# Kernel tuning notes

Hardware: AMD Instinct MI355X
Metric: run time of the kernel (lower is better)

The kernel has to match this reference:

```python
import jax, jax.numpy as jnp
import numpy as np

HIDDEN = 300
N_HEADS = 4
DEPTH = 4
N_ATOMS = 30000
N_BONDS = 60000
MAX_NB = 6
N_MOLS = 600
ATOMS_PER_MOL = 50
ATOM_FDIM = 144
BOND_IN = ATOM_FDIM + 14  # 158
W_SCALE = 0.05


def setup_inputs() -> dict:
    key = jax.random.key(0)
    ks = jax.random.split(key, 12)
    rn = lambda k, shp: jax.random.normal(k, shp, dtype=jnp.float32)
    return {
        'fatoms': rn(ks[0], (N_ATOMS, ATOM_FDIM)),
        'fbonds': rn(ks[1], (N_BONDS, BOND_IN)),
        'agraph': jax.random.randint(ks[2], (N_ATOMS, MAX_NB), 0, N_BONDS, dtype=jnp.int32),
        'bgraph': jax.random.randint(ks[3], (N_BONDS, MAX_NB), 0, N_BONDS, dtype=jnp.int32),
        'W_i': rn(ks[4], (HIDDEN, BOND_IN)) * W_SCALE,
        'W_ma': rn(ks[5], (N_HEADS, HIDDEN, HIDDEN)) * W_SCALE,
        'W_h': rn(ks[6], (HIDDEN, N_HEADS * HIDDEN)) * W_SCALE,
        'W_o': rn(ks[7], (HIDDEN, ATOM_FDIM + HIDDEN)) * W_SCALE,
        'b_o': rn(ks[8], (HIDDEN,)) * W_SCALE,
        'W_a': rn(ks[9], (HIDDEN, HIDDEN)) * W_SCALE,
        'W_b': rn(ks[10], (HIDDEN, HIDDEN)) * W_SCALE,
        'b_b': rn(ks[11], (HIDDEN,)) * W_SCALE,
    }


def reference(fatoms, fbonds, agraph, bgraph, W_i, W_ma, W_h, W_o, b_o, W_a, W_b, b_b):
    E, K = bgraph.shape
    NH = W_ma.shape[0]
    H = W_i.shape[0]

    binput = fbonds @ W_i.T                      # [E, H]
    message = jax.nn.relu(binput)
    for _ in range(DEPTH - 1):
        nei = message[bgraph]                    # [E, K, H] gather over neighbor bonds
        # per-head attention scores: <W_ma[n] @ nei_ek, message_e>
        mt = jnp.einsum('eh,nhd->ned', message, W_ma)        # [NH, E, H]
        scores = jnp.einsum('ekd,ned->nek', nei, mt)         # [NH, E, K]
        w = jax.nn.softmax(scores, axis=2)
        comp = jnp.einsum('nek,ekh->enh', w, nei)            # [E, NH, H]
        nei_msg = comp.reshape(E, NH * H) @ W_h.T            # [E, H]
        message = jax.nn.relu(binput + nei_msg)              # dropout(p=0) = identity

    a_nei = message[agraph].sum(axis=1)          # [A, H] gather-sum incoming bonds
    ainput = jnp.concatenate([fatoms, a_nei], axis=1)
    atom_hiddens = jax.nn.relu(ainput @ W_o.T + b_o)         # [A, H]

    # uniform scope: N_MOLS molecules of ATOMS_PER_MOL atoms each
    cur = atom_hiddens.reshape(N_MOLS, ATOMS_PER_MOL, H)
    att_w = jax.nn.softmax(jnp.einsum('mah,mbh->mab', cur @ W_a.T, cur), axis=2)
    att_h = jax.nn.relu(jnp.einsum('mab,mbh->mah', att_w, cur) @ W_b.T + b_b)
    mol_vecs = (cur + att_h).sum(axis=1) / ATOMS_PER_MOL     # [N_MOLS, H]
    return mol_vecs
```

## Files before the change

kernel.cpp:

```cpp
#include <hip/hip_runtime.h>
#include <hip/hip_bf16.h>
#include <math.h>

#define HID       300
#define HP        320
#define NH        4
#define E_BONDS   60000
#define NATOMS    30000
#define KNB       6
#define NMOLS     600
#define APM       50
#define AFD       144
#define BONDIN    158

typedef unsigned short u16;
typedef unsigned int   u32;
typedef _Float16 f16;
typedef f16   f16x8 __attribute__((ext_vector_type(8)));
typedef float f32x4 __attribute__((ext_vector_type(4)));

__device__ inline float hlo(u32 u) { union { u32 i; f16 h[2]; } c; c.i = u; return (float)c.h[0]; }
__device__ inline float hhi(u32 u) { union { u32 i; f16 h[2]; } c; c.i = u; return (float)c.h[1]; }
__device__ inline u32 packh2(float a, float b) {
    union { u32 i; f16 h[2]; } c; c.h[0] = (f16)a; c.h[1] = (f16)b; return c.i;
}

__device__ inline void gl2lds16(const void* g, void* l) {
    __builtin_amdgcn_global_load_lds(
        (const __attribute__((address_space(1))) void*)g,
        (__attribute__((address_space(3))) void*)l, 16, 0, 0);
}

template <int BN, int EPI>
__global__ __launch_bounds__(256, 4) void mfma_gemm_k(
    const f16* __restrict__ A, int lda,
    const f16* __restrict__ B, int ldb,
    int M, int Nb, int K, int ldc,
    int nbx, int mby,
    float* __restrict__ Cf, f16* __restrict__ Ch,
    const float* __restrict__ bias,
    const f16* __restrict__ resid,
    f16* __restrict__ out2)
{
    constexpr int NF = BN / 32;
    __shared__ f16 sA[128 * 64];
    __shared__ f16 sB[BN * 64];
    const int b    = blockIdx.x;
    const int xcd  = b & 7;
    const int q    = b >> 3;
    const int xb   = q % nbx;
    const int yb   = (q / nbx) * 8 + xcd;
    if (yb >= mby) return;
    const int tid  = threadIdx.x;
    const int lane = tid & 63;
    const int wv   = tid >> 6;
    const int wm   = wv >> 1, wn = wv & 1;
    const int m0   = yb * 128, n0 = xb * BN;

    f32x4 acc[4][NF];
#pragma unroll
    for (int i = 0; i < 4; ++i)
#pragma unroll
        for (int j = 0; j < NF; ++j) acc[i][j] = (f32x4){0.f, 0.f, 0.f, 0.f};

    for (int k0 = 0; k0 < K; k0 += 64) {
        __syncthreads();
#pragma unroll
        for (int i = 0; i < 4; ++i) {
            int o   = (((i * 4 + wv) * 64) + lane) * 16;
            int row = o >> 7;
            int p   = (o >> 4) & 7;
            int gr  = m0 + row; gr = gr < M ? gr : M - 1;
            const f16* g = A + (size_t)gr * lda + k0 + ((p ^ (row & 7)) << 3);
            gl2lds16(g, (char*)sA + (i * 4 + wv) * 1024);
        }
#pragma unroll
        for (int i = 0; i < BN / 32; ++i) {
            int o   = (((i * 4 + wv) * 64) + lane) * 16;
            int row = o >> 7;
            int p   = (o >> 4) & 7;
            int gr  = n0 + row; gr = gr < Nb ? gr : Nb - 1;
            const f16* g = B + (size_t)gr * ldb + k0 + ((p ^ (row & 7)) << 3);
            gl2lds16(g, (char*)sB + (i * 4 + wv) * 1024);
        }
        __syncthreads();

        const int rl = lane & 15, cl = lane >> 4;
#pragma unroll
        for (int kh = 0; kh < 2; ++kh) {
            f16x8 af[4], bfr[NF];
#pragma unroll
            for (int mf = 0; mf < 4; ++mf) {
                int row = wm * 64 + mf * 16 + rl;
                int ch  = (kh * 4 + cl) ^ (row & 7);
                af[mf]  = *(const f16x8*)&sA[row * 64 + ch * 8];
            }
#pragma unroll
            for (int nf = 0; nf < NF; ++nf) {
                int row = wn * (BN / 2) + nf * 16 + rl;
                int ch  = (kh * 4 + cl) ^ (row & 7);
                bfr[nf] = *(const f16x8*)&sB[row * 64 + ch * 8];
            }
#pragma unroll
            for (int mf = 0; mf < 4; ++mf)
#pragma unroll
                for (int nf = 0; nf < NF; ++nf)
                    acc[mf][nf] = __builtin_amdgcn_mfma_f32_16x16x32_f16(
                        af[mf], bfr[nf], acc[mf][nf], 0, 0, 0);
        }
    }

    const int rl = lane & 15, cl = lane >> 4;
#pragma unroll
    for (int mf = 0; mf < 4; ++mf) {
#pragma unroll
        for (int r = 0; r < 4; ++r) {
            int gm = m0 + wm * 64 + mf * 16 + cl * 4 + r;
            if (gm >= M) continue;
#pragma unroll
            for (int nf = 0; nf < NF; ++nf) {
                int gn = n0 + wn * (BN / 2) + nf * 16 + rl;
                if (gn >= ldc) continue;
                float v = acc[mf][nf][r];
                size_t ci = (size_t)gm * ldc + gn;
                if (EPI == 0) {
                    Cf[ci] = v;
                } else if (EPI == 1) {
                    Ch[ci] = (f16)v;
                } else if (EPI == 2) {
                    Ch[ci] = (f16)v;
                    out2[ci] = (f16)fmaxf(v, 0.f);
                } else if (EPI == 3) {
                    v += (float)resid[ci];
                    Ch[ci] = (f16)fmaxf(v, 0.f);
                } else if (EPI == 4) {
                    v += Cf[ci];
                    v += (gn < HID) ? bias[gn] : 0.f;
                    v = fmaxf(v, 0.f);
                    Cf[ci] = v; Ch[ci] = (f16)v;
                } else if (EPI == 5) {
                    v += (gn < HID) ? bias[gn] : 0.f;
                    Cf[ci] = fmaxf(v, 0.f);
                } else {
                    v += (gn < HID) ? bias[gn] : 0.f;
                    Ch[ci] = (f16)fmaxf(v, 0.f);
                }
            }
        }
    }
}

static inline int swz_grid(int nbx, int mby) { return nbx * 8 * ((mby + 7) / 8); }

__global__ __launch_bounds__(256) void score_comp_k(
    const f16* __restrict__ msg,
    f16* __restrict__ mtc,
    const int* __restrict__ bgraph)
{
    const int tid = threadIdx.x;
    const int e   = blockIdx.x * 16 + (tid >> 4);
    const int t   = tid & 15;

    u32 nei[KNB][10];
#pragma unroll
    for (int k = 0; k < KNB; ++k) {
        int nb = bgraph[e * KNB + k];
        const u32* p = (const u32*)(msg + (size_t)nb * HP) + t * 10;
#pragma unroll
        for (int j = 0; j < 10; ++j) nei[k][j] = p[j];
    }

    for (int n = 0; n < NH; ++n) {
        u32* mrow = (u32*)(mtc + (size_t)e * (NH * HP) + n * HP) + t * 10;
        u32 mt[10];
#pragma unroll
        for (int j = 0; j < 10; ++j) mt[j] = mrow[j];

        float pk[KNB] = {0.f, 0.f, 0.f, 0.f, 0.f, 0.f};
#pragma unroll
        for (int j = 0; j < 10; ++j) {
            float m0 = hlo(mt[j]), m1 = hhi(mt[j]);
#pragma unroll
            for (int k = 0; k < KNB; ++k)
                pk[k] += hlo(nei[k][j]) * m0 + hhi(nei[k][j]) * m1;
        }
#pragma unroll
        for (int s = 1; s < 16; s <<= 1)
#pragma unroll
            for (int k = 0; k < KNB; ++k) pk[k] += __shfl_xor(pk[k], s);

        float mx = pk[0];
#pragma unroll
        for (int k = 1; k < KNB; ++k) mx = fmaxf(mx, pk[k]);
        float w[KNB], sum = 0.f;
#pragma unroll
        for (int k = 0; k < KNB; ++k) { w[k] = __expf(pk[k] - mx); sum += w[k]; }
        float inv = 1.f / sum;
#pragma unroll
        for (int k = 0; k < KNB; ++k) w[k] *= inv;

#pragma unroll
        for (int j = 0; j < 10; ++j) {
            float c0 = 0.f, c1 = 0.f;
#pragma unroll
            for (int k = 0; k < KNB; ++k) {
                c0 += w[k] * hlo(nei[k][j]);
                c1 += w[k] * hhi(nei[k][j]);
            }
            mrow[j] = packh2(c0, c1);
        }
    }
}

__global__ void gather_sum_h_k(const f16* __restrict__ msg,
                               const int* __restrict__ agraph,
                               f16* __restrict__ out512) {
    int idx = blockIdx.x * 256 + threadIdx.x;
    if (idx >= NATOMS * (HP / 2)) return;
    int a = idx / (HP / 2), c = idx - a * (HP / 2);
    const int* g = agraph + (size_t)a * KNB;
    float s0 = 0.f, s1 = 0.f;
#pragma unroll
    for (int k = 0; k < KNB; ++k) {
        u32 u = *(const u32*)(msg + (size_t)g[k] * HP + c * 2);
        s0 += hlo(u); s1 += hhi(u);
    }
    ((u32*)out512)[(size_t)a * 256 + 96 + c] = packh2(s0, s1);
}

__global__ void conv_pad_k(const float* __restrict__ src, f16* __restrict__ dst,
                           int R, int C, int CP, int RP) {
    int idx = blockIdx.x * 256 + threadIdx.x;
    if (idx >= R * CP) return;
    int r = idx / CP, c = idx - r * CP;
    dst[(size_t)r * RP + c] = (f16)(c < C ? src[(size_t)r * C + c] : 0.f);
}

__global__ void prep_w_k(const float* __restrict__ src, f16* __restrict__ dst,
                         int mode, int R, int CK) {
    int idx = blockIdx.x * 256 + threadIdx.x;
    if (idx >= R * CK) return;
    int r = idx / CK, c = idx - r * CK;
    float v = 0.f;
    if (mode == 0) {
        if (r < HID && c < BONDIN) v = src[r * BONDIN + c];
    } else if (mode == 1) {
        int n = r / HP, d = r - n * HP;
        if (d < HID && c < HID) v = src[((size_t)n * HID + c) * HID + d];
    } else if (mode == 2) {
        int n = c / HP, d = c - n * HP;
        if (r < HID && d < HID) v = src[(size_t)r * (NH * HID) + n * HID + d];
    } else if (mode == 7) {
        if (r < HID) {
            if (c < AFD) v = src[r * (AFD + HID) + c];
            else if (c >= 192 && c < 192 + HID) v = src[r * (AFD + HID) + AFD + (c - 192)];
        }
    } else {
        if (r < HID && c < HID) v = src[r * HID + c];
    }
    dst[idx] = (f16)v;
}

__global__ __launch_bounds__(256) void mol_attn_mfma_k(
    const f16* __restrict__ atomHh,
    const f16* __restrict__ ah2h,
    f16* __restrict__ comp2h)
{
    __shared__ f16 sCur[64 * 320];
    __shared__ float sP[64][66];
    const int tid  = threadIdx.x;
    const int lane = tid & 63;
    const int wv   = tid >> 6;
    const int m    = blockIdx.x;
    const int rl   = lane & 15, cl = lane >> 4;

#pragma unroll
    for (int i = 0; i < 10; ++i) {
        int g   = i * 256 + wv * 64 + lane;
        int row = g / 40, c = g - row * 40;
        int grow = m * APM + row; grow = grow < NATOMS ? grow : NATOMS - 1;
        const f16* src = atomHh + (size_t)grow * HP + ((c ^ (row & 7)) << 3);
        gl2lds16(src, (char*)sCur + (size_t)(i * 256 + wv * 64) * 16);
    }
    __syncthreads();

    f32x4 acc[4];
#pragma unroll
    for (int nf = 0; nf < 4; ++nf) acc[nf] = (f32x4){0.f, 0.f, 0.f, 0.f};
    int qrow = m * APM + wv * 16 + rl;
    qrow = qrow < NATOMS ? qrow : NATOMS - 1;
    const f16* qbase = ah2h + (size_t)qrow * HP;
#pragma unroll
    for (int kh = 0; kh < 10; ++kh) {
        f16x8 aq = *(const f16x8*)(qbase + kh * 32 + cl * 8);
#pragma unroll
        for (int nf = 0; nf < 4; ++nf) {
            int brow = nf * 16 + rl;
            int ch   = (kh * 4 + cl) ^ (brow & 7);
            f16x8 bv = *(const f16x8*)&sCur[brow * 320 + ch * 8];
            acc[nf] = __builtin_amdgcn_mfma_f32_16x16x32_f16(aq, bv, acc[nf], 0, 0, 0);
        }
    }

#pragma unroll
    for (int r = 0; r < 4; ++r) {
        float s[4];
#pragma unroll
        for (int nf = 0; nf < 4; ++nf) {
            s[nf] = acc[nf][r];
            if (nf == 3 && rl >= 2) s[nf] = -1e30f;
        }
        float mx = fmaxf(fmaxf(s[0], s[1]), fmaxf(s[2], s[3]));
#pragma unroll
        for (int msk = 1; msk < 16; msk <<= 1) mx = fmaxf(mx, __shfl_xor(mx, msk));
        float e[4], sum = 0.f;
#pragma unroll
        for (int nf = 0; nf < 4; ++nf) { e[nf] = __expf(s[nf] - mx); sum += e[nf]; }
#pragma unroll
        for (int msk = 1; msk < 16; msk <<= 1) sum += __shfl_xor(sum, msk);
        float inv = 1.f / sum;
        int a = wv * 16 + cl * 4 + r;
#pragma unroll
        for (int nf = 0; nf < 4; ++nf) sP[a][nf * 16 + rl] = e[nf] * inv;
    }
    __syncthreads();

    const int a  = tid >> 2, hq = tid & 3;
    const bool aval = a < APM;
    const size_t orow = (size_t)(m * APM + a) * HP;
#pragma unroll
    for (int p = 0; p < 2; ++p) {
        float av[40];
#pragma unroll
        for (int i = 0; i < 40; ++i) av[i] = 0.f;
        const int ch0 = p * 20 + hq * 5;
        for (int b = 0; b < APM; ++b) {
            float w = sP[a][b];
#pragma unroll
            for (int i = 0; i < 5; ++i) {
                int ch = (ch0 + i) ^ (b & 7);
                f16x8 cv = *(const f16x8*)&sCur[b * 320 + ch * 8];
#pragma unroll
                for (int j = 0; j < 8; ++j) av[i * 8 + j] += w * (float)cv[j];
            }
        }
        if (aval) {
#pragma unroll
            for (int i = 0; i < 5; ++i) {
                f16x8 o;
#pragma unroll
                for (int j = 0; j < 8; ++j) o[j] = (f16)av[i * 8 + j];
                *(f16x8*)&comp2h[orow + p * 160 + hq * 40 + i * 8] = o;
            }
        }
    }
}

__global__ void mol_reduce_k(const f16* __restrict__ atomHh,
                             const f16* __restrict__ atthh,
                             float* __restrict__ out) {
    const int m = blockIdx.x;
    for (int h = threadIdx.x; h < HID; h += 256) {
        float s = 0.f;
        for (int a = 0; a < APM; ++a) {
            size_t i = (size_t)(m * APM + a) * HP + h;
            s += (float)atomHh[i] + (float)atthh[i];
        }
        out[(size_t)m * HID + h] = s * (1.f / APM);
    }
}

extern "C" void kernel_launch(void* const* d_in, const int* in_sizes, int n_in,
                              void* d_out, int out_size, void* d_ws, size_t ws_size,
                              hipStream_t stream) {
    const float* fatoms = (const float*)d_in[0];
    const float* fbonds = (const float*)d_in[1];
    const int*   agraph = (const int*)d_in[2];
    const int*   bgraph = (const int*)d_in[3];
    const float* W_i    = (const float*)d_in[4];
    const float* W_ma   = (const float*)d_in[5];
    const float* W_h    = (const float*)d_in[6];
    const float* W_o    = (const float*)d_in[7];
    const float* b_o    = (const float*)d_in[8];
    const float* W_a    = (const float*)d_in[9];
    const float* W_b    = (const float*)d_in[10];
    const float* b_b    = (const float*)d_in[11];
    float* out = (float*)d_out;

    char* ws = (char*)d_ws;
    f16* fbondsh = (f16*)ws;
    f16* mtall   = (f16*)ws;
    f16* fat512  = (f16*)ws;
    f16* atomHh  = (f16*)(ws + 115200000);
    f16* ah2h    = (f16*)(ws + 134400000);
    f16* comp2h  = (f16*)(ws + 153600000);
    f16* atthh   = (f16*)(ws + 172800000);
    f16* binh    = (f16*)(ws + 153600000);
    f16* msgh    = (f16*)(ws + 192000000);
    char* wb = ws + 230400000;
    f16* WiT   = (f16*)(wb);
    f16* WmaT  = (f16*)(wb + 122880);
    f16* WhT   = (f16*)(wb + 942080);
    f16* Wo512 = (f16*)(wb + 1761280);
    f16* Wa    = (f16*)(wb + 2088960);
    f16* Wb    = (f16*)(wb + 2293760);

    prep_w_k<<<dim3((320 * 192 + 255) / 256), dim3(256), 0, stream>>>(W_i, WiT, 0, 320, 192);
    prep_w_k<<<dim3((1280 * 320 + 255) / 256), dim3(256), 0, stream>>>(W_ma, WmaT, 1, 1280, 320);
    prep_w_k<<<dim3((320 * 1280 + 255) / 256), dim3(256), 0, stream>>>(W_h, WhT, 2, 320, 1280);
    prep_w_k<<<dim3((320 * 512 + 255) / 256), dim3(256), 0, stream>>>(W_o, Wo512, 7, 320, 512);
    prep_w_k<<<dim3((320 * 320 + 255) / 256), dim3(256), 0, stream>>>(W_a, Wa, 5, 320, 320);
    prep_w_k<<<dim3((320 * 320 + 255) / 256), dim3(256), 0, stream>>>(W_b, Wb, 6, 320, 320);
    conv_pad_k<<<dim3((E_BONDS * 192 + 255) / 256), dim3(256), 0, stream>>>(
        fbonds, fbondsh, E_BONDS, BONDIN, 192, 192);

    mfma_gemm_k<128, 2><<<dim3(swz_grid(3, 469)), dim3(256), 0, stream>>>(
        fbondsh, 192, WiT, 192, E_BONDS, 320, 192, HP, 3, 469,
        nullptr, binh, nullptr, nullptr, msgh);

    for (int it = 0; it < 3; ++it) {
        mfma_gemm_k<128, 1><<<dim3(swz_grid(10, 469)), dim3(256), 0, stream>>>(
            msgh, HP, WmaT, HP, E_BONDS, NH * HP, HP, NH * HP, 10, 469,
            nullptr, mtall, nullptr, nullptr, nullptr);
        score_comp_k<<<dim3(E_BONDS / 16), dim3(256), 0, stream>>>(msgh, mtall, bgraph);
        mfma_gemm_k<128, 3><<<dim3(swz_grid(3, 469)), dim3(256), 0, stream>>>(
            mtall, NH * HP, WhT, NH * HP, E_BONDS, HP, NH * HP, HP, 3, 469,
            nullptr, msgh, nullptr, binh, nullptr);
    }

    gather_sum_h_k<<<dim3((NATOMS * 160 + 255) / 256), dim3(256), 0, stream>>>(
        msgh, agraph, fat512);
    conv_pad_k<<<dim3((NATOMS * 192 + 255) / 256), dim3(256), 0, stream>>>(
        fatoms, fat512, NATOMS, AFD, 192, 512);
    mfma_gemm_k<128, 6><<<dim3(swz_grid(3, 235)), dim3(256), 0, stream>>>(
        fat512, 512, Wo512, 512, NATOMS, 320, 512, HP, 3, 235,
        nullptr, atomHh, b_o, nullptr, nullptr);

    mfma_gemm_k<128, 1><<<dim3(swz_grid(3, 235)), dim3(256), 0, stream>>>(
        atomHh, HP, Wa, HP, NATOMS, 320, HP, HP, 3, 235,
        nullptr, ah2h, nullptr, nullptr, nullptr);
    mol_attn_mfma_k<<<dim3(NMOLS), dim3(256), 0, stream>>>(atomHh, ah2h, comp2h);
    mfma_gemm_k<128, 6><<<dim3(swz_grid(3, 235)), dim3(256), 0, stream>>>(
        comp2h, HP, Wb, HP, NATOMS, 320, HP, HP, 3, 235,
        nullptr, atthh, b_b, nullptr, nullptr);
    mol_reduce_k<<<dim3(NMOLS), dim3(256), 0, stream>>>(atomHh, atthh, out);
}
```

Before: 929.6 us.

## Merge prep kernels into single launches and process two bonds per score thread

Replaces seven weight and bond conversion launches with one combined prep kernel, and fuses the atom gather-sum with the fatoms conversion into one launch, cutting launch count. The score/softmax kernel now handles two bonds per 16-lane group, with launch bounds asking for two blocks per CU, so there are half as many blocks and more independent gather loads in flight per thread. Holding neighbor data for two bonds doubles register use in that kernel, which may lower occupancy or cause spills.

```diff
diff --git a/kernel.cpp b/kernel.cpp
--- a/kernel.cpp
+++ b/kernel.cpp
@@ -152,113 +152,170 @@
 
 static inline int swz_grid(int nbx, int mby) { return nbx * 8 * ((mby + 7) / 8); }
 
-__global__ __launch_bounds__(256) void score_comp_k(
+__global__ __launch_bounds__(256, 2) void score_comp_k(
     const f16* __restrict__ msg,
     f16* __restrict__ mtc,
     const int* __restrict__ bgraph)
 {
     const int tid = threadIdx.x;
-    const int e   = blockIdx.x * 16 + (tid >> 4);
+    const int g   = tid >> 4;
     const int t   = tid & 15;
-
-    u32 nei[KNB][10];
-#pragma unroll
-    for (int k = 0; k < KNB; ++k) {
-        int nb = bgraph[e * KNB + k];
-        const u32* p = (const u32*)(msg + (size_t)nb * HP) + t * 10;
-#pragma unroll
-        for (int j = 0; j < 10; ++j) nei[k][j] = p[j];
+    const int eA  = blockIdx.x * 32 + g;
+    const int eB  = eA + 16;
+
+    u32 nei[2][KNB][10];
+#pragma unroll
+    for (int p = 0; p < 2; ++p) {
+        int e = p ? eB : eA;
+#pragma unroll
+        for (int k = 0; k < KNB; ++k) {
+            int nb = bgraph[e * KNB + k];
+            const u32* src = (const u32*)(msg + (size_t)nb * HP) + t * 10;
+#pragma unroll
+            for (int j = 0; j < 10; ++j) nei[p][k][j] = src[j];
+        }
     }
 
     for (int n = 0; n < NH; ++n) {
-        u32* mrow = (u32*)(mtc + (size_t)e * (NH * HP) + n * HP) + t * 10;
-        u32 mt[10];
-#pragma unroll
-        for (int j = 0; j < 10; ++j) mt[j] = mrow[j];
-
-        float pk[KNB] = {0.f, 0.f, 0.f, 0.f, 0.f, 0.f};
-#pragma unroll
-        for (int j = 0; j < 10; ++j) {
-            float m0 = hlo(mt[j]), m1 = hhi(mt[j]);
-#pragma unroll
-            for (int k = 0; k < KNB; ++k)
-                pk[k] += hlo(nei[k][j]) * m0 + hhi(nei[k][j]) * m1;
-        }
-#pragma unroll
-        for (int s = 1; s < 16; s <<= 1)
-#pragma unroll
-            for (int k = 0; k < KNB; ++k) pk[k] += __shfl_xor(pk[k], s);
-
-        float mx = pk[0];
-#pragma unroll
-        for (int k = 1; k < KNB; ++k) mx = fmaxf(mx, pk[k]);
-        float w[KNB], sum = 0.f;
-#pragma unroll
-        for (int k = 0; k < KNB; ++k) { w[k] = __expf(pk[k] - mx); sum += w[k]; }
-        float inv = 1.f / sum;
-#pragma unroll
-        for (int k = 0; k < KNB; ++k) w[k] *= inv;
-
-#pragma unroll
-        for (int j = 0; j < 10; ++j) {
-            float c0 = 0.f, c1 = 0.f;
-#pragma unroll
-            for (int k = 0; k < KNB; ++k) {
-                c0 += w[k] * hlo(nei[k][j]);
-                c1 += w[k] * hhi(nei[k][j]);
-            }
-            mrow[j] = packh2(c0, c1);
-        }
-    }
-}
-
-__global__ void gather_sum_h_k(const f16* __restrict__ msg,
-                               const int* __restrict__ agraph,
-                               f16* __restrict__ out512) {
+#pragma unroll
+        for (int p = 0; p < 2; ++p) {
+            int e = p ? eB : eA;
+            u32* mrow = (u32*)(mtc + (size_t)e * (NH * HP) + n * HP) + t * 10;
+            u32 mt[10];
+#pragma unroll
+            for (int j = 0; j < 10; ++j) mt[j] = mrow[j];
+
+            float pk[KNB] = {0.f, 0.f, 0.f, 0.f, 0.f, 0.f};
+#pragma unroll
+            for (int j = 0; j < 10; ++j) {
+                float m0 = hlo(mt[j]), m1 = hhi(mt[j]);
+#pragma unroll
+                for (int k = 0; k < KNB; ++k)
+                    pk[k] += hlo(nei[p][k][j]) * m0 + hhi(nei[p][k][j]) * m1;
+            }
+#pragma unroll
+            for (int s = 1; s < 16; s <<= 1)
+#pragma unroll
+                for (int k = 0; k < KNB; ++k) pk[k] += __shfl_xor(pk[k], s);
+
+            float mx = pk[0];
+#pragma unroll
+            for (int k = 1; k < KNB; ++k) mx = fmaxf(mx, pk[k]);
+            float w[KNB], sum = 0.f;
+#pragma unroll
+            for (int k = 0; k < KNB; ++k) { w[k] = __expf(pk[k] - mx); sum += w[k]; }
+            float inv = 1.f / sum;
+#pragma unroll
+            for (int k = 0; k < KNB; ++k) w[k] *= inv;
+
+#pragma unroll
+            for (int j = 0; j < 10; ++j) {
+                float c0 = 0.f, c1 = 0.f;
+#pragma unroll
+                for (int k = 0; k < KNB; ++k) {
+                    c0 += w[k] * hlo(nei[p][k][j]);
+                    c1 += w[k] * hhi(nei[p][k][j]);
+                }
+                mrow[j] = packh2(c0, c1);
+            }
+        }
+    }
+}
+
+#define S_WIT   (320 * 192)
+#define S_WMAT  (1280 * 320)
+#define S_WHT   (320 * 1280)
+#define S_WO    (320 * 512)
+#define S_WAB   (320 * 320)
+#define S_FB    (E_BONDS * 192)
+#define PREP_TOTAL (S_WIT + S_WMAT + S_WHT + S_WO + 2 * S_WAB + S_FB)
+
+__global__ void prep_all_k(
+    const float* __restrict__ W_i, const float* __restrict__ W_ma,
+    const float* __restrict__ W_h, const float* __restrict__ W_o,
+    const float* __restrict__ W_a, const float* __restrict__ W_b,
+    const float* __restrict__ fbonds,
+    f16* __restrict__ WiT, f16* __restrict__ WmaT, f16* __restrict__ WhT,
+    f16* __restrict__ Wo512, f16* __restrict__ Wa, f16* __restrict__ Wb,
+    f16* __restrict__ fbondsh)
+{
     int idx = blockIdx.x * 256 + threadIdx.x;
-    if (idx >= NATOMS * (HP / 2)) return;
-    int a = idx / (HP / 2), c = idx - a * (HP / 2);
-    const int* g = agraph + (size_t)a * KNB;
-    float s0 = 0.f, s1 = 0.f;
-#pragma unroll
-    for (int k = 0; k < KNB; ++k) {
-        u32 u = *(const u32*)(msg + (size_t)g[k] * HP + c * 2);
-        s0 += hlo(u); s1 += hhi(u);
-    }
-    ((u32*)out512)[(size_t)a * 256 + 96 + c] = packh2(s0, s1);
-}
-
-__global__ void conv_pad_k(const float* __restrict__ src, f16* __restrict__ dst,
-                           int R, int C, int CP, int RP) {
+    if (idx < S_WIT) {
+        int r = idx / 192, c = idx - r * 192;
+        WiT[idx] = (f16)((r < HID && c < BONDIN) ? W_i[r * BONDIN + c] : 0.f);
+        return;
+    }
+    idx -= S_WIT;
+    if (idx < S_WMAT) {
+        int r = idx / 320, c = idx - r * 320;
+        int n = r / HP, d = r - n * HP;
+        float v = (d < HID && c < HID) ? W_ma[((size_t)n * HID + c) * HID + d] : 0.f;
+        WmaT[idx] = (f16)v;
+        return;
+    }
+    idx -= S_WMAT;
+    if (idx < S_WHT) {
+        int r = idx / 1280, c = idx - r * 1280;
+        int n = c / HP, d = c - n * HP;
+        float v = (r < HID && d < HID) ? W_h[(size_t)r * (NH * HID) + n * HID + d] : 0.f;
+        WhT[idx] = (f16)v;
+        return;
+    }
+    idx -= S_WHT;
+    if (idx < S_WO) {
+        int r = idx / 512, c = idx - r * 512;
+        float v = 0.f;
+        if (r < HID) {
+            if (c < AFD) v = W_o[r * (AFD + HID) + c];
+            else if (c >= 192 && c < 192 + HID) v = W_o[r * (AFD + HID) + AFD + (c - 192)];
+        }
+        Wo512[idx] = (f16)v;
+        return;
+    }
+    idx -= S_WO;
+    if (idx < S_WAB) {
+        int r = idx / 320, c = idx - r * 320;
+        Wa[idx] = (f16)((r < HID && c < HID) ? W_a[r * HID + c] : 0.f);
+        return;
+    }
+    idx -= S_WAB;
+    if (idx < S_WAB) {
+        int r = idx / 320, c = idx - r * 320;
+        Wb[idx] = (f16)((r < HID && c < HID) ? W_b[r * HID + c] : 0.f);
+        return;
+    }
+    idx -= S_WAB;
+    if (idx < S_FB) {
+        int r = idx / 192, c = idx - r * 192;
+        fbondsh[idx] = (f16)(c < BONDIN ? fbonds[(size_t)r * BONDIN + c] : 0.f);
+        return;
+    }
+}
+
+__global__ void atom_prep_k(const f16* __restrict__ msg,
+                            const int* __restrict__ agraph,
+                            const float* __restrict__ fatoms,
+                            f16* __restrict__ fat512)
+{
     int idx = blockIdx.x * 256 + threadIdx.x;
-    if (idx >= R * CP) return;
-    int r = idx / CP, c = idx - r * CP;
-    dst[(size_t)r * RP + c] = (f16)(c < C ? src[(size_t)r * C + c] : 0.f);
-}
-
-__global__ void prep_w_k(const float* __restrict__ src, f16* __restrict__ dst,
-                         int mode, int R, int CK) {
-    int idx = blockIdx.x * 256 + threadIdx.x;
-    if (idx >= R * CK) return;
-    int r = idx / CK, c = idx - r * CK;
-    float v = 0.f;
-    if (mode == 0) {
-        if (r < HID && c < BONDIN) v = src[r * BONDIN + c];
-    } else if (mode == 1) {
-        int n = r / HP, d = r - n * HP;
-        if (d < HID && c < HID) v = src[((size_t)n * HID + c) * HID + d];
-    } else if (mode == 2) {
-        int n = c / HP, d = c - n * HP;
-        if (r < HID && d < HID) v = src[(size_t)r * (NH * HID) + n * HID + d];
-    } else if (mode == 7) {
-        if (r < HID) {
-            if (c < AFD) v = src[r * (AFD + HID) + c];
-            else if (c >= 192 && c < 192 + HID) v = src[r * (AFD + HID) + AFD + (c - 192)];
-        }
-    } else {
-        if (r < HID && c < HID) v = src[r * HID + c];
-    }
-    dst[idx] = (f16)v;
+    const int SA = NATOMS * (HP / 2);
+    if (idx < SA) {
+        int a = idx / (HP / 2), c = idx - a * (HP / 2);
+        const int* g = agraph + (size_t)a * KNB;
+        float s0 = 0.f, s1 = 0.f;
+#pragma unroll
+        for (int k = 0; k < KNB; ++k) {
+            u32 u = *(const u32*)(msg + (size_t)g[k] * HP + c * 2);
+            s0 += hlo(u); s1 += hhi(u);
+        }
+        ((u32*)fat512)[(size_t)a * 256 + 96 + c] = packh2(s0, s1);
+        return;
+    }
+    idx -= SA;
+    if (idx < NATOMS * 192) {
+        int r = idx / 192, c = idx - r * 192;
+        fat512[(size_t)r * 512 + c] = (f16)(c < AFD ? fatoms[(size_t)r * AFD + c] : 0.f);
+    }
 }
 
 __global__ __launch_bounds__(256) void mol_attn_mfma_k(
@@ -405,14 +462,9 @@
     f16* Wa    = (f16*)(wb + 2088960);
     f16* Wb    = (f16*)(wb + 2293760);
 
-    prep_w_k<<<dim3((320 * 192 + 255) / 256), dim3(256), 0, stream>>>(W_i, WiT, 0, 320, 192);
-    prep_w_k<<<dim3((1280 * 320 + 255) / 256), dim3(256), 0, stream>>>(W_ma, WmaT, 1, 1280, 320);
-    prep_w_k<<<dim3((320 * 1280 + 255) / 256), dim3(256), 0, stream>>>(W_h, WhT, 2, 320, 1280);
-    prep_w_k<<<dim3((320 * 512 + 255) / 256), dim3(256), 0, stream>>>(W_o, Wo512, 7, 320, 512);
-    prep_w_k<<<dim3((320 * 320 + 255) / 256), dim3(256), 0, stream>>>(W_a, Wa, 5, 320, 320);
-    prep_w_k<<<dim3((320 * 320 + 255) / 256), dim3(256), 0, stream>>>(W_b, Wb, 6, 320, 320);
-    conv_pad_k<<<dim3((E_BONDS * 192 + 255) / 256), dim3(256), 0, stream>>>(
-        fbonds, fbondsh, E_BONDS, BONDIN, 192, 192);
+    prep_all_k<<<dim3((PREP_TOTAL + 255) / 256), dim3(256), 0, stream>>>(
+        W_i, W_ma, W_h, W_o, W_a, W_b, fbonds,
+        WiT, WmaT, WhT, Wo512, Wa, Wb, fbondsh);
 
     mfma_gemm_k<128, 2><<<dim3(swz_grid(3, 469)), dim3(256), 0, stream>>>(
         fbondsh, 192, WiT, 192, E_BONDS, 320, 192, HP, 3, 469,
@@ -422,16 +474,14 @@
         mfma_gemm_k<128, 1><<<dim3(swz_grid(10, 469)), dim3(256), 0, stream>>>(
             msgh, HP, WmaT, HP, E_BONDS, NH * HP, HP, NH * HP, 10, 469,
             nullptr, mtall, nullptr, nullptr, nullptr);
-        score_comp_k<<<dim3(E_BONDS / 16), dim3(256), 0, stream>>>(msgh, mtall, bgraph);
+        score_comp_k<<<dim3(E_BONDS / 32), dim3(256), 0, stream>>>(msgh, mtall, bgraph);
         mfma_gemm_k<128, 3><<<dim3(swz_grid(3, 469)), dim3(256), 0, stream>>>(
             mtall, NH * HP, WhT, NH * HP, E_BONDS, HP, NH * HP, HP, 3, 469,
             nullptr, msgh, nullptr, binh, nullptr);
     }
 
-    gather_sum_h_k<<<dim3((NATOMS * 160 + 255) / 256), dim3(256), 0, stream>>>(
-        msgh, agraph, fat512);
-    conv_pad_k<<<dim3((NATOMS * 192 + 255) / 256), dim3(256), 0, stream>>>(
-        fatoms, fat512, NATOMS, AFD, 192, 512);
+    atom_prep_k<<<dim3((NATOMS * (HP / 2) + NATOMS * 192 + 255) / 256), dim3(256), 0, stream>>>(
+        msgh, agraph, fatoms, fat512);
     mfma_gemm_k<128, 6><<<dim3(swz_grid(3, 235)), dim3(256), 0, stream>>>(
         fat512, 512, Wo512, 512, NATOMS, 320, 512, HP, 3, 235,
         nullptr, atomHh, b_o, nullptr, nullptr);
```

New measurement: 1.067 ms. +14.7%, slower.
